# Performance work log

Hardware: AMD Instinct MI355X
Metric: run time of the kernel (lower is better)

Reference implementation:

```python
import jax, jax.numpy as jnp
import numpy as np

B, NPG, FANOUT = 32, 1024, 4       # graphs, nodes per graph, tree fan-out
H = 128                            # x_size == h_size
NUM_LAYERS = 4
A, BCAPS = 8, 8                    # TreeCaps a, b
DCC, N_CLASSES = 16, 50
ROUTING_ITER = 3
TYPE_VOCAB, TOKEN_VOCAB = 1000, 30000
EPS = 1e-10


def _build_forest():
    # parent of node i (i>0) is (i-1)//FANOUT; node 0 is root. Same tree per graph.
    child = np.arange(1, NPG)
    parent = (child - 1) // FANOUT
    pos = ((child - 1) % FANOUT).astype(np.float32)           # position in parent's mailbox
    cnt = np.bincount(parent, minlength=NPG).astype(np.float32)
    k = cnt[parent]                                           # child count of each edge's parent
    denom = np.maximum(k - 1.0, 1.0)
    lw = np.where(k == 1.0, 1.0, (k - 1.0 - pos) / denom).astype(np.float32)
    rw = np.where(k == 1.0, 0.0, pos / denom).astype(np.float32)
    offs = (np.arange(B) * NPG)[:, None]
    src = (child[None, :] + offs).reshape(-1).astype(np.int32)
    dst = (parent[None, :] + offs).reshape(-1).astype(np.int32)
    return src, dst, np.tile(lw, B), np.tile(rw, B), np.tile(cnt > 0, B)


def setup_inputs() -> dict:
    key = jax.random.key(0)
    ks = jax.random.split(key, 9)
    src, dst, lw, rw, has_children = _build_forest()
    N = B * NPG
    u = lambda k, s: jax.random.uniform(k, s, jnp.float32, -0.1, 0.1)
    return {
        "type_ids": jax.random.randint(ks[0], (N,), 0, TYPE_VOCAB, dtype=jnp.int32),
        "token_ids": jax.random.randint(ks[1], (N,), 0, TOKEN_VOCAB, dtype=jnp.int32),
        "src": jnp.asarray(src), "dst": jnp.asarray(dst),
        "lw": jnp.asarray(lw), "rw": jnp.asarray(rw),
        "has_children": jnp.asarray(has_children),
        "type_emb": jax.random.normal(ks[2], (TYPE_VOCAB, H - H // 2), jnp.float32),
        "token_emb": jax.random.normal(ks[3], (TOKEN_VOCAB, H // 2), jnp.float32),
        "W_left": u(ks[4], (NUM_LAYERS, H, H)),
        "W_right": u(ks[5], (NUM_LAYERS, H, H)),
        "W_top": u(ks[6], (NUM_LAYERS, H, H)),
        "b_conv": u(ks[7], (NUM_LAYERS, H)),
        "Wjm": 0.01 * jax.random.normal(ks[8], (A * H, DCC, N_CLASSES, NUM_LAYERS), jnp.float32),
    }


def squash(x, axis=-1):
    sq = jnp.sum(x * x, axis=axis, keepdims=True)
    return x * (sq / (1.0 + sq) / (jnp.sqrt(sq + EPS) + 1e-8))


def _vts_routing(uu):
    # uu: [NPG, H, L]  (one graph's primary capsules)
    l2 = jnp.sum(uu.reshape(NPG, -1) ** 2, axis=1)
    _, top_b = jax.lax.top_k(l2, BCAPS)
    u_i = jax.lax.stop_gradient(uu[top_b].reshape(-1, NUM_LAYERS))  # [BCAPS*H, L]
    _, top_a = jax.lax.top_k(l2, A)
    v_j = uu[top_a].reshape(-1, NUM_LAYERS)                         # [A*H, L]
    alpha = jnp.zeros((BCAPS * H, A * H), uu.dtype)
    for _ in range(ROUTING_ITER):
        alpha = alpha + u_i @ v_j.T
        beta = jax.nn.softmax(alpha, axis=-1)
        v_j = beta.T @ u_i
    return squash(v_j)                                              # [A*H, L]


def _dynamic_routing(SC, Wjm):
    # SC: [B, A*H, L], Wjm: [A*H, DCC, S, L]
    v = jnp.einsum('ncsm,bnm->bnsc', Wjm, SC)
    v_stop = jax.lax.stop_gradient(v)
    delta = jnp.zeros(SC.shape[:2] + (N_CLASSES,), SC.dtype)
    z = None
    for r in range(ROUTING_ITER):
        gamma = jax.nn.softmax(delta, axis=-1)
        vv = v if r == ROUTING_ITER - 1 else v_stop
        z = squash(jnp.einsum('bns,bnsc->bsc', gamma, vv))
        if r < ROUTING_ITER - 1:
            delta = delta + jnp.einsum('bnsc,bsc->bns', v_stop, z)
    return z                                                        # [B, S, DCC]


def reference(type_ids, token_ids, src, dst, lw, rw, has_children,
              type_emb, token_emb, W_left, W_right, W_top, b_conv, Wjm):
    h = jnp.concatenate([type_emb[type_ids], token_emb[token_ids]], axis=1)  # [N, H]
    N = h.shape[0]
    feats = []
    for l in range(NUM_LAYERS):
        ch = h[src]                                                 # [E, H] gather children
        msg = (ch @ W_left[l]) * lw[:, None] + (ch @ W_right[l]) * rw[:, None]
        children = jax.ops.segment_sum(msg, dst, num_segments=N)
        new_h = jax.nn.relu(children + h @ W_top[l] + b_conv[l][None, :])
        h = jnp.where(has_children[:, None], new_h, h)              # leaves keep old h
        feats.append(h)
    layer_feats = jnp.stack(feats, axis=-1)                         # [N, H, L]
    SC = jax.vmap(_vts_routing)(layer_feats.reshape(B, NPG, H, NUM_LAYERS))
    z = _dynamic_routing(SC, Wjm)
    logit = jnp.sqrt(jnp.sum(z * z, axis=-1) + EPS)                 # [B, S]
    return (logit, logit)
```

## Files before the change

### kernel.cpp

```cpp
#include <hip/hip_runtime.h>


#define BG      32
#define NPG     1024
#define HH      128
#define NLAY    4
#define INT_PG  256
#define M_INT   8192
#define NN      32768
#define EPG     1023
#define DCC     16
#define NS      50

__global__ void k_embed(const int* __restrict__ tids, const int* __restrict__ kids,
                        const float* __restrict__ temb, const float* __restrict__ kemb,
                        float* __restrict__ h) {
  int idx = blockIdx.x * 256 + threadIdx.x;
  int n = idx >> 5, c4 = idx & 31;
  float4 v;
  if (c4 < 16) v = *(const float4*)(temb + tids[n] * 64 + c4 * 4);
  else         v = *(const float4*)(kemb + kids[n] * 64 + (c4 - 16) * 4);
  *(float4*)(h + n * 128 + c4 * 4) = v;
}

__global__ void k_gather(const float* __restrict__ h, const int* __restrict__ src,
                         const float* __restrict__ lw, const float* __restrict__ rw,
                         float* __restrict__ hl, float* __restrict__ hr) {
  int idx = blockIdx.x * 256 + threadIdx.x;
  int p = idx >> 5, c4 = idx & 31;
  int g = p >> 8, pl = p & 255;
  float4 al = make_float4(0.f, 0.f, 0.f, 0.f);
  float4 ar = make_float4(0.f, 0.f, 0.f, 0.f);
  for (int j = 0; j < 4; ++j) {
    int cc = 4 * pl + 1 + j;
    if (cc < NPG) {
      int e = g * EPG + cc - 1;
      int child = src[e];
      float lv = lw[e], rv = rw[e];
      float4 hv = *(const float4*)(h + child * 128 + c4 * 4);
      al.x = fmaf(lv, hv.x, al.x); al.y = fmaf(lv, hv.y, al.y);
      al.z = fmaf(lv, hv.z, al.z); al.w = fmaf(lv, hv.w, al.w);
      ar.x = fmaf(rv, hv.x, ar.x); ar.y = fmaf(rv, hv.y, ar.y);
      ar.z = fmaf(rv, hv.z, ar.z); ar.w = fmaf(rv, hv.w, ar.w);
    }
  }
  *(float4*)(hl + p * 128 + c4 * 4) = al;
  *(float4*)(hr + p * 128 + c4 * 4) = ar;
}

__global__ __launch_bounds__(256) void k_conv(
    const float* __restrict__ hl, const float* __restrict__ hr,
    float* __restrict__ h,
    const float* __restrict__ Wl, const float* __restrict__ Wr,
    const float* __restrict__ Wt, const float* __restrict__ bias,
    float* __restrict__ feat) {
  __shared__ float Ws[32][128];
  __shared__ float AsT[32][40];
  int tid = threadIdx.x;
  int tx = tid & 31, ty = tid >> 5;
  int rowBase = blockIdx.x * 32;
  int nodeBase = ((rowBase >> 8) << 10) + (rowBase & 255);
  float acc[4][4] = {};
  int sr = tid >> 3, sc4 = (tid & 7) * 4;

  for (int kc = 0; kc < 12; ++kc) {
    int ssel = kc >> 2, kcol = (kc & 3) * 32;
    const float* ap = (ssel == 0) ? (hl + rowBase * 128)
                    : (ssel == 1) ? (hr + rowBase * 128)
                                  : (h + nodeBase * 128);
    const float* wsrc = ((ssel == 0) ? Wl : (ssel == 1) ? Wr : Wt) + kcol * 128;
    float4 av = *(const float4*)(ap + sr * 128 + kcol + sc4);
    float4 wv0, wv1, wv2, wv3;
    {
      int f0 = tid, f1 = tid + 256, f2 = tid + 512, f3 = tid + 768;
      wv0 = *(const float4*)(wsrc + (f0 >> 5) * 128 + (f0 & 31) * 4);
      wv1 = *(const float4*)(wsrc + (f1 >> 5) * 128 + (f1 & 31) * 4);
      wv2 = *(const float4*)(wsrc + (f2 >> 5) * 128 + (f2 & 31) * 4);
      wv3 = *(const float4*)(wsrc + (f3 >> 5) * 128 + (f3 & 31) * 4);
    }
    __syncthreads();
    AsT[sc4 + 0][sr] = av.x; AsT[sc4 + 1][sr] = av.y;
    AsT[sc4 + 2][sr] = av.z; AsT[sc4 + 3][sr] = av.w;
    {
      int f0 = tid, f1 = tid + 256, f2 = tid + 512, f3 = tid + 768;
      *(float4*)&Ws[f0 >> 5][(f0 & 31) * 4] = wv0;
      *(float4*)&Ws[f1 >> 5][(f1 & 31) * 4] = wv1;
      *(float4*)&Ws[f2 >> 5][(f2 & 31) * 4] = wv2;
      *(float4*)&Ws[f3 >> 5][(f3 & 31) * 4] = wv3;
    }
    __syncthreads();
    #pragma unroll
    for (int kk = 0; kk < 32; ++kk) {
      float4 wv = *(float4*)&Ws[kk][tx * 4];
      float4 av2 = *(float4*)&AsT[kk][ty * 4];
      float aa[4] = {av2.x, av2.y, av2.z, av2.w};
      float ww[4] = {wv.x, wv.y, wv.z, wv.w};
      #pragma unroll
      for (int i = 0; i < 4; ++i)
        #pragma unroll
        for (int j = 0; j < 4; ++j)
          acc[i][j] = fmaf(aa[i], ww[j], acc[i][j]);
    }
  }
  float4 bv = *(const float4*)(bias + tx * 4);
  float bb[4] = {bv.x, bv.y, bv.z, bv.w};
  #pragma unroll
  for (int i = 0; i < 4; ++i) {
    int r = ty * 4 + i;
    float4 o = make_float4(fmaxf(acc[i][0] + bb[0], 0.f),
                           fmaxf(acc[i][1] + bb[1], 0.f),
                           fmaxf(acc[i][2] + bb[2], 0.f),
                           fmaxf(acc[i][3] + bb[3], 0.f));
    *(float4*)(feat + (rowBase + r) * 128 + tx * 4) = o;
    *(float4*)(h + (nodeBase + r) * 128 + tx * 4) = o;
  }
}

__global__ void k_l2(const float* __restrict__ h, const float* __restrict__ feat,
                     float* __restrict__ l2) {
  int wid = (blockIdx.x * 256 + threadIdx.x) >> 6;
  int lane = threadIdx.x & 63;
  int g = wid >> 10, local = wid & 1023;
  float s = 0.f;
  if (local >= INT_PG) {
    const float* p = h + wid * 128;
    float a = p[lane], b = p[lane + 64];
    s = (a * a + b * b) * 4.f;
  } else {
    int row = (g * INT_PG + local) * 128;
    #pragma unroll
    for (int l = 0; l < 4; ++l) {
      const float* p = feat + l * (M_INT * 128) + row;
      float a = p[lane], b = p[lane + 64];
      s += a * a + b * b;
    }
  }
  #pragma unroll
  for (int off = 32; off; off >>= 1) s += __shfl_down(s, off);
  if (lane == 0) l2[wid] = s;
}

__global__ void k_topk(const float* __restrict__ l2, int* __restrict__ sel) {
  __shared__ unsigned long long keys[1024];
  __shared__ unsigned long long red[256];
  int g = blockIdx.x, tid = threadIdx.x;
  for (int i = tid; i < 1024; i += 256) {
    unsigned vb = __float_as_uint(l2[g * 1024 + i]);
    keys[i] = ((unsigned long long)vb << 32) | (unsigned)(~i);
  }
  __syncthreads();
  for (int r = 0; r < 8; ++r) {
    unsigned long long best = 0ULL;
    for (int i = tid; i < 1024; i += 256) {
      unsigned long long k = keys[i];
      best = (k > best) ? k : best;
    }
    red[tid] = best;
    __syncthreads();
    for (int st = 128; st; st >>= 1) {
      if (tid < st) {
        unsigned long long a = red[tid], b = red[tid + st];
        red[tid] = (b > a) ? b : a;
      }
      __syncthreads();
    }
    if (tid == 0) {
      unsigned long long k = red[0];
      int idx = (int)(~(unsigned)(k & 0xffffffffu));
      sel[g * 8 + r] = idx;
      keys[idx] = 0ULL;
    }
    __syncthreads();
  }
}

__global__ void k_buildU(const float* __restrict__ h, const float* __restrict__ feat,
                         const int* __restrict__ sel,
                         float* __restrict__ U, float* __restrict__ Vsum) {
  int idx = blockIdx.x * 256 + threadIdx.x;
  int g = idx >> 10, rank = (idx >> 7) & 7, hh = idx & 127;
  int local = sel[g * 8 + rank];
  float4 v;
  if (local >= INT_PG) {
    float x = h[(g * NPG + local) * 128 + hh];
    v = make_float4(x, x, x, x);
  } else {
    int row = (g * INT_PG + local) * 128 + hh;
    v.x = feat[row];
    v.y = feat[M_INT * 128 + row];
    v.z = feat[2 * M_INT * 128 + row];
    v.w = feat[3 * M_INT * 128 + row];
  }
  int o = g * 1024 + rank * 128 + hh;
  ((float4*)U)[o] = v;
  ((float4*)Vsum)[o] = v;
}

__global__ __launch_bounds__(1024) void k_vtsA(const float* __restrict__ U,
                                               const float* __restrict__ Vsum,
                                               float* __restrict__ mw, float* __restrict__ sw) {
  __shared__ float4 Vs[1024];
  __shared__ float2 red[1024];
  int g = blockIdx.x >> 3, rb = (blockIdx.x & 7) * 128;
  int tid = threadIdx.x, l = tid & 63, p = tid >> 6;
  Vs[tid] = ((const float4*)Vsum)[g * 1024 + tid];
  __syncthreads();
  float4 u0 = ((const float4*)U)[g * 1024 + rb + l];
  float4 u1 = ((const float4*)U)[g * 1024 + rb + 64 + l];
  int j0 = p * 64;
  float m0 = -3.4e38f, m1 = -3.4e38f;
  for (int j = j0; j < j0 + 64; ++j) {
    float4 v = Vs[j];
    float a0 = u0.x * v.x + u0.y * v.y + u0.z * v.z + u0.w * v.w;
    float a1 = u1.x * v.x + u1.y * v.y + u1.z * v.z + u1.w * v.w;
    m0 = fmaxf(m0, a0); m1 = fmaxf(m1, a1);
  }
  red[tid] = make_float2(m0, m1);
  __syncthreads();
  #pragma unroll
  for (int st = 512; st >= 64; st >>= 1) {
    if (tid < st) {
      float2 a = red[tid], b = red[tid + st];
      red[tid] = make_float2(fmaxf(a.x, b.x), fmaxf(a.y, b.y));
    }
    __syncthreads();
  }
  float2 mm = red[l];
  __syncthreads();
  float s0 = 0.f, s1 = 0.f;
  for (int j = j0; j < j0 + 64; ++j) {
    float4 v = Vs[j];
    float a0 = u0.x * v.x + u0.y * v.y + u0.z * v.z + u0.w * v.w;
    float a1 = u1.x * v.x + u1.y * v.y + u1.z * v.z + u1.w * v.w;
    s0 += __expf(a0 - mm.x);
    s1 += __expf(a1 - mm.y);
  }
  red[tid] = make_float2(s0, s1);
  __syncthreads();
  #pragma unroll
  for (int st = 512; st >= 64; st >>= 1) {
    if (tid < st) {
      float2 a = red[tid], b = red[tid + st];
      red[tid] = make_float2(a.x + b.x, a.y + b.y);
    }
    __syncthreads();
  }
  if (tid < 64) {
    float2 ss = red[tid];
    mw[g * 1024 + rb + tid] = mm.x;
    mw[g * 1024 + rb + 64 + tid] = mm.y;
    sw[g * 1024 + rb + tid] = ss.x;
    sw[g * 1024 + rb + 64 + tid] = ss.y;
  }
}

__global__ __launch_bounds__(1024) void k_vtsB(const float* __restrict__ U,
                                               float* __restrict__ Vsum,
                                               const float* __restrict__ mw,
                                               const float* __restrict__ sw,
                                               float* __restrict__ SCT, int last) {
  __shared__ float4 Us[1024];
  __shared__ float2 ms[1024];
  __shared__ float4 par[1024];
  int g = blockIdx.x >> 3, cb = (blockIdx.x & 7) * 128;
  int tid = threadIdx.x, l = tid & 63, p = tid >> 6;
  Us[tid] = ((const float4*)U)[g * 1024 + tid];
  ms[tid] = make_float2(mw[g * 1024 + tid], 1.0f / sw[g * 1024 + tid]);
  __syncthreads();
  float4 v0 = ((const float4*)Vsum)[g * 1024 + cb + l];
  float4 v1 = ((const float4*)Vsum)[g * 1024 + cb + 64 + l];
  float4 acc0 = make_float4(0.f, 0.f, 0.f, 0.f);
  float4 acc1 = make_float4(0.f, 0.f, 0.f, 0.f);
  int i0 = p * 64;
  for (int i = i0; i < i0 + 64; ++i) {
    float4 uu = Us[i];
    float2 st = ms[i];
    float a0 = uu.x * v0.x + uu.y * v0.y + uu.z * v0.z + uu.w * v0.w;
    float a1 = uu.x * v1.x + uu.y * v1.y + uu.z * v1.z + uu.w * v1.w;
    float w0 = __expf(a0 - st.x) * st.y;
    float w1 = __expf(a1 - st.x) * st.y;
    acc0.x = fmaf(w0, uu.x, acc0.x); acc0.y = fmaf(w0, uu.y, acc0.y);
    acc0.z = fmaf(w0, uu.z, acc0.z); acc0.w = fmaf(w0, uu.w, acc0.w);
    acc1.x = fmaf(w1, uu.x, acc1.x); acc1.y = fmaf(w1, uu.y, acc1.y);
    acc1.z = fmaf(w1, uu.z, acc1.z); acc1.w = fmaf(w1, uu.w, acc1.w);
  }
  par[tid] = acc0;
  __syncthreads();
  #pragma unroll
  for (int st = 512; st >= 64; st >>= 1) {
    if (tid < st) {
      float4 a = par[tid], b = par[tid + st];
      par[tid] = make_float4(a.x + b.x, a.y + b.y, a.z + b.z, a.w + b.w);
    }
    __syncthreads();
  }
  float4 o0;
  if (tid < 64) o0 = par[tid];
  __syncthreads();
  par[tid] = acc1;
  __syncthreads();
  #pragma unroll
  for (int st = 512; st >= 64; st >>= 1) {
    if (tid < st) {
      float4 a = par[tid], b = par[tid + st];
      par[tid] = make_float4(a.x + b.x, a.y + b.y, a.z + b.z, a.w + b.w);
    }
    __syncthreads();
  }
  if (tid < 64) {
    float4 o1 = par[tid];
    int j0c = cb + tid, j1c = cb + 64 + tid;
    if (last) {
      float sq0 = o0.x * o0.x + o0.y * o0.y + o0.z * o0.z + o0.w * o0.w;
      float f0 = (sq0 / (1.f + sq0)) / (sqrtf(sq0 + 1e-10f) + 1e-8f);
      ((float4*)SCT)[j0c * 32 + g] = make_float4(o0.x * f0, o0.y * f0, o0.z * f0, o0.w * f0);
      float sq1 = o1.x * o1.x + o1.y * o1.y + o1.z * o1.z + o1.w * o1.w;
      float f1 = (sq1 / (1.f + sq1)) / (sqrtf(sq1 + 1e-10f) + 1e-8f);
      ((float4*)SCT)[j1c * 32 + g] = make_float4(o1.x * f1, o1.y * f1, o1.z * f1, o1.w * f1);
    } else {
      float4 w0 = ((const float4*)Vsum)[g * 1024 + j0c];
      float4 w1 = ((const float4*)Vsum)[g * 1024 + j1c];
      ((float4*)Vsum)[g * 1024 + j0c] = make_float4(w0.x + o0.x, w0.y + o0.y,
                                                    w0.z + o0.z, w0.w + o0.w);
      ((float4*)Vsum)[g * 1024 + j1c] = make_float4(w1.x + o1.x, w1.y + o1.y,
                                                    w1.z + o1.z, w1.w + o1.w);
    }
  }
}

__global__ void k_transW(const float* __restrict__ Wjm, float* __restrict__ WT) {
  __shared__ float w[3200];
  int n = blockIdx.x, tid = threadIdx.x;
  for (int i = tid; i < 3200; i += 256) w[i] = Wjm[n * 3200 + i];
  __syncthreads();
  for (int i = tid; i < 3200; i += 256) {
    int s = i >> 6, cm = i & 63, cc = cm >> 2, m = cm & 3;
    WT[(s * 1024 + n) * 64 + cm] = w[(cc * NS + s) * 4 + m];
  }
}

__global__ void k_gamma(const float* __restrict__ delta, float* __restrict__ gT) {
  int idx = blockIdx.x * 256 + threadIdx.x;
  int b = idx & 31, n = idx >> 5;
  const float* dp = delta + n * 32 + b;
  float m = -3.4e38f;
  for (int s = 0; s < NS; ++s) m = fmaxf(m, dp[s * 32768]);
  float sum = 0.f;
  for (int s = 0; s < NS; ++s) sum += __expf(dp[s * 32768] - m);
  float inv = 1.0f / sum;
  float* gp = gT + n * 32 + b;
  for (int s = 0; s < NS; ++s) gp[s * 32768] = __expf(dp[s * 32768] - m) * inv;
}

__global__ __launch_bounds__(256) void k_zsweep(const float* __restrict__ WT,
                                                const float* __restrict__ SCT,
                                                const float* __restrict__ gT,
                                                float* __restrict__ accZ, int it0) {
  int sb = blockIdx.x >> 3, nb = blockIdx.x & 7;
  int tid = threadIdx.x;
  int b = tid & 31, ch = tid >> 5;
  int n0 = nb * 128;
  const float4* wt = (const float4*)WT + (sb * 1024 + n0) * 16;
  const float4* sct = (const float4*)SCT + n0 * 32 + b;
  const float* gp = gT + (sb * 1024 + n0) * 32 + b;
  float a0 = 0.f, a1 = 0.f;
  for (int nn = 0; nn < 128; ++nn) {
    float4 w0 = wt[nn * 16 + ch];
    float4 w1 = wt[nn * 16 + ch + 8];
    float4 s4 = sct[nn * 32];
    float gm = it0 ? (1.0f / 50.0f) : gp[nn * 32];
    float t0 = w0.x * s4.x + w0.y * s4.y + w0.z * s4.z + w0.w * s4.w;
    float t1 = w1.x * s4.x + w1.y * s4.y + w1.z * s4.z + w1.w * s4.w;
    a0 = fmaf(gm, t0, a0);
    a1 = fmaf(gm, t1, a1);
  }
  atomicAdd(accZ + (b * NS + sb) * 16 + ch, a0);
  atomicAdd(accZ + (b * NS + sb) * 16 + ch + 8, a1);
}

__global__ void k_squash(const float* __restrict__ accZ, float* __restrict__ z,
                         float* __restrict__ out, int fin) {
  int idx = blockIdx.x * 256 + threadIdx.x;
  if (idx >= 1600) return;
  const float4* a4 = (const float4*)accZ + idx * 4;
  float4 u0 = a4[0], u1 = a4[1], u2 = a4[2], u3 = a4[3];
  float sq = u0.x * u0.x + u0.y * u0.y + u0.z * u0.z + u0.w * u0.w
           + u1.x * u1.x + u1.y * u1.y + u1.z * u1.z + u1.w * u1.w
           + u2.x * u2.x + u2.y * u2.y + u2.z * u2.z + u2.w * u2.w
           + u3.x * u3.x + u3.y * u3.y + u3.z * u3.z + u3.w * u3.w;
  float f = (sq / (1.f + sq)) / (sqrtf(sq + 1e-10f) + 1e-8f);
  if (fin) {
    float lg = sqrtf(sq * f * f + 1e-10f);
    out[idx] = lg;
    out[idx + 1600] = lg;
  } else {
    float4* z4 = (float4*)z + idx * 4;
    z4[0] = make_float4(u0.x * f, u0.y * f, u0.z * f, u0.w * f);
    z4[1] = make_float4(u1.x * f, u1.y * f, u1.z * f, u1.w * f);
    z4[2] = make_float4(u2.x * f, u2.y * f, u2.z * f, u2.w * f);
    z4[3] = make_float4(u3.x * f, u3.y * f, u3.z * f, u3.w * f);
  }
}

__global__ __launch_bounds__(256) void k_dsweep(const float* __restrict__ WT,
                                                const float* __restrict__ SCT,
                                                const float* __restrict__ z,
                                                float* __restrict__ delta, int first) {
  __shared__ float wl[50 * 64];
  __shared__ float4 scl[32];
  int n = blockIdx.x;
  int tid = threadIdx.x;
  for (int i = tid; i < 3200; i += 256)
    wl[i] = WT[((i >> 6) * 1024 + n) * 64 + (i & 63)];
  if (tid < 32) scl[tid] = ((const float4*)SCT)[n * 32 + tid];
  __syncthreads();
  for (int idx = tid; idx < 1600; idx += 256) {
    int s = idx >> 5, b = idx & 31;
    const float4* wp = (const float4*)(wl + s * 64);
    const float4* zp = (const float4*)(z + (b * 50 + s) * 16);
    float4 z0 = zp[0], z1 = zp[1], z2 = zp[2], z3 = zp[3];
    float zs[16] = {z0.x, z0.y, z0.z, z0.w, z1.x, z1.y, z1.z, z1.w,
                    z2.x, z2.y, z2.z, z2.w, z3.x, z3.y, z3.z, z3.w};
    float4 y = make_float4(0.f, 0.f, 0.f, 0.f);
    #pragma unroll
    for (int c = 0; c < 16; ++c) {
      float4 w = wp[c];
      float zc = zs[c];
      y.x = fmaf(zc, w.x, y.x); y.y = fmaf(zc, w.y, y.y);
      y.z = fmaf(zc, w.z, y.z); y.w = fmaf(zc, w.w, y.w);
    }
    float4 sc = scl[b];
    float dd = sc.x * y.x + sc.y * y.y + sc.z * y.z + sc.w * y.w;
    float* dp = delta + (s * 1024 + n) * 32 + b;
    if (first) *dp = dd; else *dp = *dp + dd;
  }
}

extern "C" void kernel_launch(void* const* d_in, const int* in_sizes, int n_in,
                              void* d_out, int out_size, void* d_ws, size_t ws_size,
                              hipStream_t stream) {
  const int*   type_ids  = (const int*)d_in[0];
  const int*   token_ids = (const int*)d_in[1];
  const int*   src       = (const int*)d_in[2];
  const float* lw        = (const float*)d_in[4];
  const float* rw        = (const float*)d_in[5];
  const float* temb      = (const float*)d_in[7];
  const float* kemb      = (const float*)d_in[8];
  const float* Wl        = (const float*)d_in[9];
  const float* Wr        = (const float*)d_in[10];
  const float* Wt        = (const float*)d_in[11];
  const float* bconv     = (const float*)d_in[12];
  const float* Wjm       = (const float*)d_in[13];
  float* out = (float*)d_out;
  char* wsb = (char*)d_ws;

  float* h     = (float*)(wsb + 0);
  float* WT    = (float*)(wsb + 0);
  float* feat  = (float*)(wsb + 16777216);
  float* gT    = (float*)(wsb + 16777216);
  float* delta = (float*)(wsb + 23330816);
  float* accZ  = (float*)(wsb + 29884416);
  float* zbuf  = (float*)(wsb + 29986816);
  float* hl    = (float*)(wsb + 33554432);
  float* hr    = (float*)(wsb + 37748736);
  float* l2b   = (float*)(wsb + 33554432);
  int*   sel   = (int*)  (wsb + 33685504);
  float* U     = (float*)(wsb + 33686528);
  float* Vsum  = (float*)(wsb + 34210816);
  float* mw    = (float*)(wsb + 34735104);
  float* sw    = (float*)(wsb + 34866176);
  float* SCT   = (float*)(wsb + 34997248);

  k_embed<<<4096, 256, 0, stream>>>(type_ids, token_ids, temb, kemb, h);

  for (int l = 0; l < NLAY; ++l) {
    k_gather<<<1024, 256, 0, stream>>>(h, src, lw, rw, hl, hr);
    k_conv<<<256, 256, 0, stream>>>(hl, hr, h,
                                    Wl + l * 16384, Wr + l * 16384, Wt + l * 16384,
                                    bconv + l * 128, feat + l * (M_INT * 128));
  }

  k_l2<<<8192, 256, 0, stream>>>(h, feat, l2b);
  k_topk<<<32, 256, 0, stream>>>(l2b, sel);
  k_buildU<<<128, 256, 0, stream>>>(h, feat, sel, U, Vsum);
  k_transW<<<1024, 256, 0, stream>>>(Wjm, WT);

  for (int it = 0; it < 3; ++it) {
    k_vtsA<<<256, 1024, 0, stream>>>(U, Vsum, mw, sw);
    k_vtsB<<<256, 1024, 0, stream>>>(U, Vsum, mw, sw, SCT, it == 2 ? 1 : 0);
  }

  for (int it = 0; it < 3; ++it) {
    if (it > 0) k_gamma<<<128, 256, 0, stream>>>(delta, gT);
    hipMemsetAsync(accZ, 0, 32 * 50 * 16 * 4, stream);
    k_zsweep<<<400, 256, 0, stream>>>(WT, SCT, gT, accZ, it == 0 ? 1 : 0);
    k_squash<<<7, 256, 0, stream>>>(accZ, zbuf, out, it == 2 ? 1 : 0);
    if (it < 2) k_dsweep<<<1024, 256, 0, stream>>>(WT, SCT, zbuf, delta, it == 0 ? 1 : 0);
  }
}
```

Before: 514.4 us.

## Fuse child gather into conv, ping-pong h, warp top-k, fuse squash into dsweep

The child gather is folded into the conv kernel through shared-memory staging, and node state is double-buffered (hA/hB) so layers read the previous state and write the next. Top-k becomes a per-wavefront register reduction with four graphs per block instead of a block-wide shared-memory tree. The squash is recomputed inside dsweep so the separate squash kernel and z buffer go away, with the logits computed once at the end. Also included: gamma caches its values in registers, zsweep uses finer blocks with unrolling, and transW is moved earlier. These cut kernel launches and intermediate global traffic, at the cost of more shared memory per conv block and a larger workspace.

```diff
diff --git a/kernel.cpp b/kernel.cpp
--- a/kernel.cpp
+++ b/kernel.cpp
@@ -14,62 +14,70 @@
 
 __global__ void k_embed(const int* __restrict__ tids, const int* __restrict__ kids,
                         const float* __restrict__ temb, const float* __restrict__ kemb,
-                        float* __restrict__ h) {
+                        float* __restrict__ hA, float* __restrict__ hB) {
   int idx = blockIdx.x * 256 + threadIdx.x;
   int n = idx >> 5, c4 = idx & 31;
   float4 v;
   if (c4 < 16) v = *(const float4*)(temb + tids[n] * 64 + c4 * 4);
   else         v = *(const float4*)(kemb + kids[n] * 64 + (c4 - 16) * 4);
-  *(float4*)(h + n * 128 + c4 * 4) = v;
-}
-
-__global__ void k_gather(const float* __restrict__ h, const int* __restrict__ src,
-                         const float* __restrict__ lw, const float* __restrict__ rw,
-                         float* __restrict__ hl, float* __restrict__ hr) {
-  int idx = blockIdx.x * 256 + threadIdx.x;
-  int p = idx >> 5, c4 = idx & 31;
-  int g = p >> 8, pl = p & 255;
-  float4 al = make_float4(0.f, 0.f, 0.f, 0.f);
-  float4 ar = make_float4(0.f, 0.f, 0.f, 0.f);
-  for (int j = 0; j < 4; ++j) {
-    int cc = 4 * pl + 1 + j;
-    if (cc < NPG) {
-      int e = g * EPG + cc - 1;
-      int child = src[e];
-      float lv = lw[e], rv = rw[e];
-      float4 hv = *(const float4*)(h + child * 128 + c4 * 4);
-      al.x = fmaf(lv, hv.x, al.x); al.y = fmaf(lv, hv.y, al.y);
-      al.z = fmaf(lv, hv.z, al.z); al.w = fmaf(lv, hv.w, al.w);
-      ar.x = fmaf(rv, hv.x, ar.x); ar.y = fmaf(rv, hv.y, ar.y);
-      ar.z = fmaf(rv, hv.z, ar.z); ar.w = fmaf(rv, hv.w, ar.w);
-    }
-  }
-  *(float4*)(hl + p * 128 + c4 * 4) = al;
-  *(float4*)(hr + p * 128 + c4 * 4) = ar;
+  *(float4*)(hA + n * 128 + c4 * 4) = v;
+  if ((n & 1023) >= INT_PG)
+    *(float4*)(hB + n * 128 + c4 * 4) = v;
 }
 
 __global__ __launch_bounds__(256) void k_conv(
-    const float* __restrict__ hl, const float* __restrict__ hr,
-    float* __restrict__ h,
+    const float* __restrict__ hp, float* __restrict__ hn,
+    const int* __restrict__ src, const float* __restrict__ lw,
+    const float* __restrict__ rw,
     const float* __restrict__ Wl, const float* __restrict__ Wr,
     const float* __restrict__ Wt, const float* __restrict__ bias,
     float* __restrict__ feat) {
   __shared__ float Ws[32][128];
   __shared__ float AsT[32][40];
+  __shared__ float hlS[32][128];
+  __shared__ float hrS[32][128];
   int tid = threadIdx.x;
   int tx = tid & 31, ty = tid >> 5;
   int rowBase = blockIdx.x * 32;
-  int nodeBase = ((rowBase >> 8) << 10) + (rowBase & 255);
+  int g = rowBase >> 8, plBase = rowBase & 255;
+  int nodeBase = g * NPG + plBase;
+
+  #pragma unroll
+  for (int t = 0; t < 4; ++t) {
+    int it = tid + t * 256;
+    int pw = it >> 5, c4 = it & 31;
+    int pl = plBase + pw;
+    float4 al = make_float4(0.f, 0.f, 0.f, 0.f);
+    float4 ar = make_float4(0.f, 0.f, 0.f, 0.f);
+    #pragma unroll
+    for (int j = 0; j < 4; ++j) {
+      int cc = 4 * pl + 1 + j;
+      if (cc < NPG) {
+        int e = g * EPG + cc - 1;
+        int child = src[e];
+        float lv = lw[e], rv = rw[e];
+        float4 hv = *(const float4*)(hp + child * 128 + c4 * 4);
+        al.x = fmaf(lv, hv.x, al.x); al.y = fmaf(lv, hv.y, al.y);
+        al.z = fmaf(lv, hv.z, al.z); al.w = fmaf(lv, hv.w, al.w);
+        ar.x = fmaf(rv, hv.x, ar.x); ar.y = fmaf(rv, hv.y, ar.y);
+        ar.z = fmaf(rv, hv.z, ar.z); ar.w = fmaf(rv, hv.w, ar.w);
+      }
+    }
+    *(float4*)&hlS[pw][c4 * 4] = al;
+    *(float4*)&hrS[pw][c4 * 4] = ar;
+  }
+  __syncthreads();
+
   float acc[4][4] = {};
   int sr = tid >> 3, sc4 = (tid & 7) * 4;
 
   for (int kc = 0; kc < 12; ++kc) {
     int ssel = kc >> 2, kcol = (kc & 3) * 32;
-    const float* ap = (ssel == 0) ? (hl + rowBase * 128)
-                    : (ssel == 1) ? (hr + rowBase * 128)
-                                  : (h + nodeBase * 128);
+    float4 av;
+    if (ssel == 0)      av = *(const float4*)&hlS[sr][kcol + sc4];
+    else if (ssel == 1) av = *(const float4*)&hrS[sr][kcol + sc4];
+    else                av = *(const float4*)(hp + (nodeBase + sr) * 128 + kcol + sc4);
     const float* wsrc = ((ssel == 0) ? Wl : (ssel == 1) ? Wr : Wt) + kcol * 128;
-    float4 av = *(const float4*)(ap + sr * 128 + kcol + sc4);
     float4 wv0, wv1, wv2, wv3;
     {
       int f0 = tid, f1 = tid + 256, f2 = tid + 512, f3 = tid + 768;
@@ -112,7 +120,7 @@
                            fmaxf(acc[i][2] + bb[2], 0.f),
                            fmaxf(acc[i][3] + bb[3], 0.f));
     *(float4*)(feat + (rowBase + r) * 128 + tx * 4) = o;
-    *(float4*)(h + (nodeBase + r) * 128 + tx * 4) = o;
+    *(float4*)(hn + (nodeBase + r) * 128 + tx * 4) = o;
   }
 }
 
@@ -140,37 +148,30 @@
   if (lane == 0) l2[wid] = s;
 }
 
-__global__ void k_topk(const float* __restrict__ l2, int* __restrict__ sel) {
-  __shared__ unsigned long long keys[1024];
-  __shared__ unsigned long long red[256];
-  int g = blockIdx.x, tid = threadIdx.x;
-  for (int i = tid; i < 1024; i += 256) {
+__global__ __launch_bounds__(256) void k_topk(const float* __restrict__ l2,
+                                              int* __restrict__ sel) {
+  int w = threadIdx.x >> 6, lane = threadIdx.x & 63;
+  int g = blockIdx.x * 4 + w;
+  unsigned long long kk[16];
+  #pragma unroll
+  for (int k = 0; k < 16; ++k) {
+    int i = k * 64 + lane;
     unsigned vb = __float_as_uint(l2[g * 1024 + i]);
-    keys[i] = ((unsigned long long)vb << 32) | (unsigned)(~i);
-  }
-  __syncthreads();
+    kk[k] = ((unsigned long long)vb << 32) | (unsigned)(~i);
+  }
   for (int r = 0; r < 8; ++r) {
     unsigned long long best = 0ULL;
-    for (int i = tid; i < 1024; i += 256) {
-      unsigned long long k = keys[i];
-      best = (k > best) ? k : best;
-    }
-    red[tid] = best;
-    __syncthreads();
-    for (int st = 128; st; st >>= 1) {
-      if (tid < st) {
-        unsigned long long a = red[tid], b = red[tid + st];
-        red[tid] = (b > a) ? b : a;
-      }
-      __syncthreads();
-    }
-    if (tid == 0) {
-      unsigned long long k = red[0];
-      int idx = (int)(~(unsigned)(k & 0xffffffffu));
-      sel[g * 8 + r] = idx;
-      keys[idx] = 0ULL;
-    }
-    __syncthreads();
+    #pragma unroll
+    for (int k = 0; k < 16; ++k) best = (kk[k] > best) ? kk[k] : best;
+    #pragma unroll
+    for (int off = 32; off; off >>= 1) {
+      unsigned long long o = __shfl_down(best, off);
+      best = (o > best) ? o : best;
+    }
+    best = __shfl(best, 0);
+    if (lane == 0) sel[g * 8 + r] = (int)(~(unsigned)(best & 0xffffffffu));
+    #pragma unroll
+    for (int k = 0; k < 16; ++k) if (kk[k] == best) kk[k] = 0ULL;
   }
 }
 
@@ -334,7 +335,8 @@
   for (int i = tid; i < 3200; i += 256) w[i] = Wjm[n * 3200 + i];
   __syncthreads();
   for (int i = tid; i < 3200; i += 256) {
-    int s = i >> 6, cm = i & 63, cc = cm >> 2, m = cm & 3;
+    int s = i >> 6, cm = i & 63;
+    int cc = cm >> 2, m = cm & 3;
     WT[(s * 1024 + n) * 64 + cm] = w[(cc * NS + s) * 4 + m];
   }
 }
@@ -343,28 +345,33 @@
   int idx = blockIdx.x * 256 + threadIdx.x;
   int b = idx & 31, n = idx >> 5;
   const float* dp = delta + n * 32 + b;
+  float d[NS];
   float m = -3.4e38f;
-  for (int s = 0; s < NS; ++s) m = fmaxf(m, dp[s * 32768]);
+  #pragma unroll
+  for (int s = 0; s < NS; ++s) { d[s] = dp[s * 32768]; m = fmaxf(m, d[s]); }
   float sum = 0.f;
-  for (int s = 0; s < NS; ++s) sum += __expf(dp[s * 32768] - m);
+  #pragma unroll
+  for (int s = 0; s < NS; ++s) { d[s] = __expf(d[s] - m); sum += d[s]; }
   float inv = 1.0f / sum;
   float* gp = gT + n * 32 + b;
-  for (int s = 0; s < NS; ++s) gp[s * 32768] = __expf(dp[s * 32768] - m) * inv;
+  #pragma unroll
+  for (int s = 0; s < NS; ++s) gp[s * 32768] = d[s] * inv;
 }
 
 __global__ __launch_bounds__(256) void k_zsweep(const float* __restrict__ WT,
                                                 const float* __restrict__ SCT,
                                                 const float* __restrict__ gT,
                                                 float* __restrict__ accZ, int it0) {
-  int sb = blockIdx.x >> 3, nb = blockIdx.x & 7;
+  int sb = blockIdx.x >> 4, nb = blockIdx.x & 15;
   int tid = threadIdx.x;
   int b = tid & 31, ch = tid >> 5;
-  int n0 = nb * 128;
+  int n0 = nb * 64;
   const float4* wt = (const float4*)WT + (sb * 1024 + n0) * 16;
   const float4* sct = (const float4*)SCT + n0 * 32 + b;
   const float* gp = gT + (sb * 1024 + n0) * 32 + b;
   float a0 = 0.f, a1 = 0.f;
-  for (int nn = 0; nn < 128; ++nn) {
+  #pragma unroll 4
+  for (int nn = 0; nn < 64; ++nn) {
     float4 w0 = wt[nn * 16 + ch];
     float4 w1 = wt[nn * 16 + ch + 8];
     float4 s4 = sct[nn * 32];
@@ -378,8 +385,7 @@
   atomicAdd(accZ + (b * NS + sb) * 16 + ch + 8, a1);
 }
 
-__global__ void k_squash(const float* __restrict__ accZ, float* __restrict__ z,
-                         float* __restrict__ out, int fin) {
+__global__ void k_logits(const float* __restrict__ accZ, float* __restrict__ out) {
   int idx = blockIdx.x * 256 + threadIdx.x;
   if (idx >= 1600) return;
   const float4* a4 = (const float4*)accZ + idx * 4;
@@ -389,22 +395,14 @@
            + u2.x * u2.x + u2.y * u2.y + u2.z * u2.z + u2.w * u2.w
            + u3.x * u3.x + u3.y * u3.y + u3.z * u3.z + u3.w * u3.w;
   float f = (sq / (1.f + sq)) / (sqrtf(sq + 1e-10f) + 1e-8f);
-  if (fin) {
-    float lg = sqrtf(sq * f * f + 1e-10f);
-    out[idx] = lg;
-    out[idx + 1600] = lg;
-  } else {
-    float4* z4 = (float4*)z + idx * 4;
-    z4[0] = make_float4(u0.x * f, u0.y * f, u0.z * f, u0.w * f);
-    z4[1] = make_float4(u1.x * f, u1.y * f, u1.z * f, u1.w * f);
-    z4[2] = make_float4(u2.x * f, u2.y * f, u2.z * f, u2.w * f);
-    z4[3] = make_float4(u3.x * f, u3.y * f, u3.z * f, u3.w * f);
-  }
+  float lg = sqrtf(sq * f * f + 1e-10f);
+  out[idx] = lg;
+  out[idx + 1600] = lg;
 }
 
 __global__ __launch_bounds__(256) void k_dsweep(const float* __restrict__ WT,
                                                 const float* __restrict__ SCT,
-                                                const float* __restrict__ z,
+                                                const float* __restrict__ accZ,
                                                 float* __restrict__ delta, int first) {
   __shared__ float wl[50 * 64];
   __shared__ float4 scl[32];
@@ -417,10 +415,17 @@
   for (int idx = tid; idx < 1600; idx += 256) {
     int s = idx >> 5, b = idx & 31;
     const float4* wp = (const float4*)(wl + s * 64);
-    const float4* zp = (const float4*)(z + (b * 50 + s) * 16);
-    float4 z0 = zp[0], z1 = zp[1], z2 = zp[2], z3 = zp[3];
-    float zs[16] = {z0.x, z0.y, z0.z, z0.w, z1.x, z1.y, z1.z, z1.w,
-                    z2.x, z2.y, z2.z, z2.w, z3.x, z3.y, z3.z, z3.w};
+    const float4* zp = (const float4*)(accZ + (b * 50 + s) * 16);
+    float4 u0 = zp[0], u1 = zp[1], u2 = zp[2], u3 = zp[3];
+    float sq = u0.x * u0.x + u0.y * u0.y + u0.z * u0.z + u0.w * u0.w
+             + u1.x * u1.x + u1.y * u1.y + u1.z * u1.z + u1.w * u1.w
+             + u2.x * u2.x + u2.y * u2.y + u2.z * u2.z + u2.w * u2.w
+             + u3.x * u3.x + u3.y * u3.y + u3.z * u3.z + u3.w * u3.w;
+    float f = (sq / (1.f + sq)) / (sqrtf(sq + 1e-10f) + 1e-8f);
+    float zs[16] = {u0.x * f, u0.y * f, u0.z * f, u0.w * f,
+                    u1.x * f, u1.y * f, u1.z * f, u1.w * f,
+                    u2.x * f, u2.y * f, u2.z * f, u2.w * f,
+                    u3.x * f, u3.y * f, u3.z * f, u3.w * f};
     float4 y = make_float4(0.f, 0.f, 0.f, 0.f);
     #pragma unroll
     for (int c = 0; c < 16; ++c) {
@@ -454,36 +459,35 @@
   float* out = (float*)d_out;
   char* wsb = (char*)d_ws;
 
-  float* h     = (float*)(wsb + 0);
-  float* WT    = (float*)(wsb + 0);
-  float* feat  = (float*)(wsb + 16777216);
-  float* gT    = (float*)(wsb + 16777216);
-  float* delta = (float*)(wsb + 23330816);
-  float* accZ  = (float*)(wsb + 29884416);
-  float* zbuf  = (float*)(wsb + 29986816);
-  float* hl    = (float*)(wsb + 33554432);
-  float* hr    = (float*)(wsb + 37748736);
-  float* l2b   = (float*)(wsb + 33554432);
-  int*   sel   = (int*)  (wsb + 33685504);
-  float* U     = (float*)(wsb + 33686528);
-  float* Vsum  = (float*)(wsb + 34210816);
-  float* mw    = (float*)(wsb + 34735104);
-  float* sw    = (float*)(wsb + 34866176);
-  float* SCT   = (float*)(wsb + 34997248);
-
-  k_embed<<<4096, 256, 0, stream>>>(type_ids, token_ids, temb, kemb, h);
+  float* hA    = (float*)(wsb + 0);
+  float* hB    = (float*)(wsb + 16777216);
+  float* feat  = (float*)(wsb + 33554432);
+  float* WT    = (float*)(wsb + 50331648);
+  float* delta = (float*)(wsb + 63963136);
+  float* gT    = (float*)(wsb + 71303168);
+  float* accZ  = (float*)(wsb + 78643200);
+  float* l2b   = (float*)(wsb + 78774272);
+  int*   sel   = (int*)  (wsb + 78905344);
+  float* U     = (float*)(wsb + 78909440);
+  float* Vsum  = (float*)(wsb + 79433728);
+  float* mw    = (float*)(wsb + 79958016);
+  float* sw    = (float*)(wsb + 80089088);
+  float* SCT   = (float*)(wsb + 80220160);
+
+  k_embed<<<4096, 256, 0, stream>>>(type_ids, token_ids, temb, kemb, hA, hB);
+  k_transW<<<1024, 256, 0, stream>>>(Wjm, WT);
 
   for (int l = 0; l < NLAY; ++l) {
-    k_gather<<<1024, 256, 0, stream>>>(h, src, lw, rw, hl, hr);
-    k_conv<<<256, 256, 0, stream>>>(hl, hr, h,
+    const float* hp = (l & 1) ? hB : hA;
+    float*       hn = (l & 1) ? hA : hB;
+    k_conv<<<256, 256, 0, stream>>>(hp, hn, src, lw, rw,
                                     Wl + l * 16384, Wr + l * 16384, Wt + l * 16384,
                                     bconv + l * 128, feat + l * (M_INT * 128));
   }
 
-  k_l2<<<8192, 256, 0, stream>>>(h, feat, l2b);
-  k_topk<<<32, 256, 0, stream>>>(l2b, sel);
-  k_buildU<<<128, 256, 0, stream>>>(h, feat, sel, U, Vsum);
-  k_transW<<<1024, 256, 0, stream>>>(Wjm, WT);
+  k_l2<<<8192, 256, 0, stream>>>(hA, feat, l2b);
+  k_topk<<<8, 256, 0, stream>>>(l2b, sel);
+  k_buildU<<<128, 256, 0, stream>>>(hA, feat, sel, U, Vsum);
 
   for (int it = 0; it < 3; ++it) {
     k_vtsA<<<256, 1024, 0, stream>>>(U, Vsum, mw, sw);
@@ -493,8 +497,8 @@
   for (int it = 0; it < 3; ++it) {
     if (it > 0) k_gamma<<<128, 256, 0, stream>>>(delta, gT);
     hipMemsetAsync(accZ, 0, 32 * 50 * 16 * 4, stream);
-    k_zsweep<<<400, 256, 0, stream>>>(WT, SCT, gT, accZ, it == 0 ? 1 : 0);
-    k_squash<<<7, 256, 0, stream>>>(accZ, zbuf, out, it == 2 ? 1 : 0);
-    if (it < 2) k_dsweep<<<1024, 256, 0, stream>>>(WT, SCT, zbuf, delta, it == 0 ? 1 : 0);
-  }
-}
+    k_zsweep<<<800, 256, 0, stream>>>(WT, SCT, gT, accZ, it == 0 ? 1 : 0);
+    if (it < 2) k_dsweep<<<1024, 256, 0, stream>>>(WT, SCT, accZ, delta, it == 0 ? 1 : 0);
+  }
+  k_logits<<<7, 256, 0, stream>>>(accZ, out);
+}
```

Measured after the change: 523.7 us. No clear change (+1.8%).
